# Optimization experiments

Measured on AMD Instinct MI355X. Metric: run time of the kernel, lower is better.

The kernel has to match this reference:

```python
import jax, jax.numpy as jnp
import numpy as np

IDIM = 128   # idim == odim (fc1 input dim must match shift-slice width idim_q)
HDIM = 1024
CDIM = 256
IGNORE_OUT = 10000.0


def setup_inputs() -> dict:
    key = jax.random.key(0)
    ks = jax.random.split(key, 4)
    B, T = 4, 512
    x = jax.random.normal(ks[0], (B, T, IDIM), dtype=jnp.float32)
    y = jax.random.normal(ks[1], (B, T, IDIM), dtype=jnp.float32)
    # xavier-ish init for the two linears (bias zeroed, as in initialize())
    w1 = jax.random.normal(ks[2], (HDIM, IDIM), dtype=jnp.float32) / np.sqrt(IDIM).astype(np.float32)
    b1 = jnp.zeros((HDIM,), jnp.float32)
    w2 = jax.random.normal(ks[3], (IDIM, HDIM), dtype=jnp.float32) / np.sqrt(HDIM).astype(np.float32)
    b2 = jnpts = jnp.zeros((IDIM,), jnp.float32)
    return {"x": x, "y": y, "w1": w1, "b1": b1, "w2": w2, "b2": b2}


def _shift_stack(key_seq, idim):
    """Vectorized _pad_for_shift: (B,T,idim) -> (B,T,2*idim-1,idim) shifted slices."""
    pad = idim - 1
    kp = jnp.pad(key_seq, ((0, 0), (0, 0), (pad, pad)))  # (B,T,3*idim-2)
    idx = jnp.arange(2 * idim - 1)[:, None] + jnp.arange(idim)[None, :]  # (S, idim)
    return kp[..., idx]  # (B,T,S,idim)


def _forward(x, y, w1, b1, w2, b2):
    idim = IDIM
    n_iter = HDIM // CDIM
    seq_mask = (y == IGNORE_OUT)                      # (B,T,odim)
    denom = jnp.sum(~seq_mask).astype(x.dtype)
    y_res, x_res = y, x
    losses = []
    for i in range(n_iter):
        # --- argaug (scale=False): sliding cosine cross-correlation + argmax ---
        kpt = _shift_stack(x_res, idim)               # (B,T,S,idim), S=2*idim-1
        num = jnp.einsum('btd,btsd->bts', y_res, kpt)
        den = jnp.linalg.norm(y_res, axis=-1)[..., None] * jnp.linalg.norm(kpt, axis=-1)
        sim = jnp.where(den == 0, 0.0, num / jnp.where(den == 0, 1.0, den))  # NaN(0/0) -> 0
        idx = jnp.argmax(sim, axis=-1)                # (B,T), first max like torch.max
        x_aug = jnp.take_along_axis(kpt, idx[..., None, None], axis=2)[..., 0, :]  # (B,T,idim)
        # --- attention (detached) ---
        attn = jax.lax.stop_gradient(jax.nn.softmax(x_aug * y_res, axis=-1))
        x_attn = x_aug * attn
        # --- _reverse_pad_for_shift: un-shift x_attn by 2*idim-2 - idx ---
        pad = idim - 1
        xap = jnp.pad(x_attn, ((0, 0), (0, 0), (pad, pad)))
        ridx = (2 * idim - 2 - idx)[..., None] + jnp.arange(idim)  # (B,T,idim)
        x_ele = jnp.take_along_axis(xap, ridx, axis=-1)
        # --- channel-masked two-layer MLP ---
        h = x_attn @ w1.T + b1                        # (B,T,hdim)
        m = jnp.zeros((HDIM,), x.dtype).at[i * CDIM:(i + 1) * CDIM].set(1.0)
        y_ele = (h * m) @ w2.T + b2                   # (B,T,odim)
        # --- masked MSE (sum of masked squared errors / #unmasked) ---
        sq = jnp.where(seq_mask, 0.0, (y_ele - y_res) ** 2)
        losses.append(jnp.sum(sq) / denom)
        y_res = y_res - y_ele
        x_res = x_res - x_ele
    return jnp.mean(jnp.stack(losses))


def reference(x, y, w1, b1, w2, b2):
    return _forward(x, y, w1, b1, w2, b2)
```

## Files before the change

kernel.cpp:

```cpp
#include <hip/hip_runtime.h>
#include <math.h>

#define NBLK  2048
#define NITER 4
#define IGNORE_OUT 10000.0f
#define LOG2E 1.44269504088896340736f

__device__ __forceinline__ float readlanef(float v, int lane){
  return __int_as_float(__builtin_amdgcn_readlane(__float_as_int(v), lane));
}

__device__ __forceinline__ float waveScanInc(float v){
  v += __int_as_float(__builtin_amdgcn_update_dpp(0, __float_as_int(v), 0x111, 0xF, 0xF, true));
  v += __int_as_float(__builtin_amdgcn_update_dpp(0, __float_as_int(v), 0x112, 0xF, 0xF, true));
  v += __int_as_float(__builtin_amdgcn_update_dpp(0, __float_as_int(v), 0x114, 0xF, 0xF, true));
  v += __int_as_float(__builtin_amdgcn_update_dpp(0, __float_as_int(v), 0x118, 0xF, 0xF, true));
  v += __int_as_float(__builtin_amdgcn_update_dpp(0, __float_as_int(v), 0x142, 0xA, 0xF, true));
  v += __int_as_float(__builtin_amdgcn_update_dpp(0, __float_as_int(v), 0x143, 0xC, 0xF, true));
  return v;
}
__device__ __forceinline__ float waveSum(float v){
  return readlanef(waveScanInc(v), 63);
}
__device__ __forceinline__ void waveArgmax(float &v, int &i){
#define AMSTEP(ctrl, rm) { \
    float ov = __int_as_float(__builtin_amdgcn_update_dpp(__float_as_int(v), __float_as_int(v), ctrl, rm, 0xF, false)); \
    int   oi = __builtin_amdgcn_update_dpp(i, i, ctrl, rm, 0xF, false); \
    bool take = (ov > v) || (ov == v && oi < i); \
    v = take ? ov : v; i = take ? oi : i; }
  AMSTEP(0x111, 0xF) AMSTEP(0x112, 0xF) AMSTEP(0x114, 0xF)
  AMSTEP(0x118, 0xF) AMSTEP(0x142, 0xA) AMSTEP(0x143, 0xC)
#undef AMSTEP
  v = readlanef(v, 63);
  i = __builtin_amdgcn_readlane(i, 63);
}
__device__ __forceinline__ void gatherPair(float v0, float v1, int idx, float &a, float &b){
  int c = idx & 63;
  float g0 = __shfl(v0, c, 64);
  float g1 = __shfl(v1, c, 64);
  a = ((unsigned)idx < 128u) ? ((idx & 64) ? g1 : g0) : 0.f;
  int idx2 = idx + 64;
  b = ((unsigned)idx2 < 128u) ? ((idx2 & 64) ? g1 : g0) : 0.f;
}

__global__ __launch_bounds__(256)
void prepK(const float* __restrict__ w1, const float* __restrict__ b1,
           const float* __restrict__ w2, const float* __restrict__ b2,
           float* __restrict__ M4, float* __restrict__ biasT, int* __restrict__ ticket){
  const int blk = blockIdx.x;
  const int tid = threadIdx.x;
  const int u = tid & 127, h = tid >> 7;
  __shared__ float part[256];
  if (blk < 512){
    int i = blk >> 7, o = blk & 127;
    const float* w1p = w1 + (i * 256 + h * 128) * 128 + u;
    const float* w2p = w2 + o * 1024 + i * 256 + h * 128;
    float a0 = 0.f, a1 = 0.f, a2 = 0.f, a3 = 0.f;
    #pragma unroll 8
    for (int c = 0; c < 128; c += 4){
      a0 = fmaf(w1p[(c + 0) * 128], w2p[c + 0], a0);
      a1 = fmaf(w1p[(c + 1) * 128], w2p[c + 1], a1);
      a2 = fmaf(w1p[(c + 2) * 128], w2p[c + 2], a2);
      a3 = fmaf(w1p[(c + 3) * 128], w2p[c + 3], a3);
    }
    part[tid] = (a0 + a1) + (a2 + a3);
    __syncthreads();
    if (h == 0) M4[i * 16384 + (u >> 2) * 512 + o * 4 + (u & 3)] = part[u] + part[128 + u];
  } else if (blk < 516){
    int i = blk - 512;
    const float* w2p = w2 + u * 1024 + i * 256 + h * 128;
    const float* b1p = b1 + i * 256 + h * 128;
    float a0 = h ? 0.f : b2[u], a1 = 0.f, a2 = 0.f, a3 = 0.f;
    #pragma unroll 8
    for (int c = 0; c < 128; c += 4){
      a0 = fmaf(b1p[c + 0], w2p[c + 0], a0);
      a1 = fmaf(b1p[c + 1], w2p[c + 1], a1);
      a2 = fmaf(b1p[c + 2], w2p[c + 2], a2);
      a3 = fmaf(b1p[c + 3], w2p[c + 3], a3);
    }
    part[tid] = (a0 + a1) + (a2 + a3);
    __syncthreads();
    if (h == 0) biasT[i * 128 + u] = part[u] + part[128 + u];
  } else {
    if (tid == 0) *ticket = 0;
  }
}

#define MLD(d0, d1, d2, d3, gg) \
  d0 = Mp[((gg) * 4 + 0) * 128 + u]; d1 = Mp[((gg) * 4 + 1) * 128 + u]; \
  d2 = Mp[((gg) * 4 + 2) * 128 + u]; d3 = Mp[((gg) * 4 + 3) * 128 + u];
#define MFM(m0, m1, m2, m3, src, kb) \
  a0 = fmaf((m0).x, readlanef(src, (kb) + 0), a0);  a0 = fmaf((m0).y, readlanef(src, (kb) + 1), a0); \
  a0 = fmaf((m0).z, readlanef(src, (kb) + 2), a0);  a0 = fmaf((m0).w, readlanef(src, (kb) + 3), a0); \
  a1 = fmaf((m1).x, readlanef(src, (kb) + 4), a1);  a1 = fmaf((m1).y, readlanef(src, (kb) + 5), a1); \
  a1 = fmaf((m1).z, readlanef(src, (kb) + 6), a1);  a1 = fmaf((m1).w, readlanef(src, (kb) + 7), a1); \
  a2 = fmaf((m2).x, readlanef(src, (kb) + 8), a2);  a2 = fmaf((m2).y, readlanef(src, (kb) + 9), a2); \
  a2 = fmaf((m2).z, readlanef(src, (kb) +10), a2);  a2 = fmaf((m2).w, readlanef(src, (kb) +11), a2); \
  a3 = fmaf((m3).x, readlanef(src, (kb) +12), a3);  a3 = fmaf((m3).y, readlanef(src, (kb) +13), a3); \
  a3 = fmaf((m3).z, readlanef(src, (kb) +14), a3);  a3 = fmaf((m3).w, readlanef(src, (kb) +15), a3);

__global__ __launch_bounds__(128, 4)
void mainK(const float* __restrict__ x, const float* __restrict__ y,
           const float* __restrict__ M4, const float* __restrict__ biasT,
           unsigned long long* __restrict__ partials, int* __restrict__ ticket,
           float* __restrict__ out){
  __shared__ float yd[384];
  __shared__ float sVal[2];
  __shared__ int   sIdx[2];
  __shared__ float sL[2], sC[2];
  __shared__ int   sOld;

  const int u = threadIdx.x;
  const int l = u & 63;
  const int w = u >> 6;
  const long base = (long)blockIdx.x * 128;

  float xlo = x[base + l], xhi = x[base + 64 + l];
  float ylo = y[base + l], yhi = y[base + 64 + l];
  const float yOwn0 = w ? yhi : ylo;
  const bool mOwn = (yOwn0 == IGNORE_OUT);
  float cnt = mOwn ? 0.f : 1.f;
  float lossAcc = 0.f;

  yd[128 + u] = yOwn0; yd[256 + u] = yOwn0;
  __syncthreads();

  for (int i = 0; i < NITER; ++i){
    const float4* Mp = (const float4*)(M4 + (size_t)i * 16384);

    float own2 = w ? xhi * xhi : xlo * xlo;
    float oth2 = w ? xlo * xlo : xhi * xhi;
    float v = waveScanInc(own2);
    float osum  = waveSum(oth2);
    float total = readlanef(v, 63) + osum;
    float pref_t = w ? (v + osum) : v;
    float ny2 = waveSum(ylo * ylo + yhi * yhi);

    const float* wp = yd + (255 - u);
    float s0=0.f,s1=0.f,s2=0.f,s3=0.f;
    float t0=0.f,t1=0.f,t2=0.f,t3=0.f;
    float p0=0.f,p1=0.f,p2=0.f,p3=0.f;
    if (w == 0){
      #pragma unroll
      for (int j = 0; j < 64; j += 4){
        float wv0 = wp[j], wv1 = wp[j+1], wv2 = wp[j+2], wv3 = wp[j+3];
        float x0 = readlanef(xlo, j),   x1 = readlanef(xlo, j+1);
        float x2 = readlanef(xlo, j+2), x3 = readlanef(xlo, j+3);
        s0 = fmaf(wv0, x0, s0); s1 = fmaf(wv1, x1, s1);
        s2 = fmaf(wv2, x2, s2); s3 = fmaf(wv3, x3, s3);
        p0 = fmaf((l >= j    ) ? wv0 : 0.f, x0, p0);
        p1 = fmaf((l >= j + 1) ? wv1 : 0.f, x1, p1);
        p2 = fmaf((l >= j + 2) ? wv2 : 0.f, x2, p2);
        p3 = fmaf((l >= j + 3) ? wv3 : 0.f, x3, p3);
      }
      #pragma unroll
      for (int j = 0; j < 64; j += 4){
        float wv0 = wp[64+j], wv1 = wp[64+j+1], wv2 = wp[64+j+2], wv3 = wp[64+j+3];
        t0 = fmaf(wv0, readlanef(xhi, j),   t0);
        t1 = fmaf(wv1, readlanef(xhi, j+1), t1);
        t2 = fmaf(wv2, readlanef(xhi, j+2), t2);
        t3 = fmaf(wv3, readlanef(xhi, j+3), t3);
      }
    } else {
      #pragma unroll
      for (int j = 0; j < 64; j += 4){
        float wv0 = wp[j], wv1 = wp[j+1], wv2 = wp[j+2], wv3 = wp[j+3];
        s0 = fmaf(wv0, readlanef(xlo, j),   s0);
        s1 = fmaf(wv1, readlanef(xlo, j+1), s1);
        s2 = fmaf(wv2, readlanef(xlo, j+2), s2);
        s3 = fmaf(wv3, readlanef(xlo, j+3), s3);
      }
      #pragma unroll
      for (int j = 0; j < 64; j += 4){
        float wv0 = wp[64+j], wv1 = wp[64+j+1], wv2 = wp[64+j+2], wv3 = wp[64+j+3];
        float x0 = readlanef(xhi, j),   x1 = readlanef(xhi, j+1);
        float x2 = readlanef(xhi, j+2), x3 = readlanef(xhi, j+3);
        t0 = fmaf(wv0, x0, t0); t1 = fmaf(wv1, x1, t1);
        t2 = fmaf(wv2, x2, t2); t3 = fmaf(wv3, x3, t3);
        p0 = fmaf((l >= j    ) ? wv0 : 0.f, x0, p0);
        p1 = fmaf((l >= j + 1) ? wv1 : 0.f, x1, p1);
        p2 = fmaf((l >= j + 2) ? wv2 : 0.f, x2, p2);
        p3 = fmaf((l >= j + 3) ? wv3 : 0.f, x3, p3);
      }
    }
    float Sh0 = (s0 + s1) + (s2 + s3);
    float Sh1 = (t0 + t1) + (t2 + t3);
    float P   = (p0 + p1) + (p2 + p3);
    float nt = Sh0 + Sh1;
    float n1 = w ? (Sh0 + P) : P;

    {
      bool yz = (ny2 == 0.f);
      float rNY = __builtin_amdgcn_rsqf(ny2);
      float nx2b = fmaxf(total - pref_t, 0.f);
      float s1v = (yz || pref_t == 0.f) ? 0.f : n1 * __builtin_amdgcn_rsqf(pref_t) * rNY;
      float s2v = (yz || nx2b  == 0.f) ? 0.f : (nt - n1) * __builtin_amdgcn_rsqf(nx2b) * rNY;
      if (u == 127) s2v = -INFINITY;
      float bv = s1v; int bi = u;
      if (s2v > bv){ bv = s2v; bi = u + 128; }
      waveArgmax(bv, bi);
      if (l == 0){ sVal[w] = bv; sIdx[w] = bi; }
    }
    __syncthreads();

    float4 A0, A1, A2, A3, B0, B1, B2, B3;
    MLD(A0, A1, A2, A3, 0)
    MLD(B0, B1, B2, B3, 1)
    float bias_i = biasT[i * 128 + u];

    int sstar;
    {
      float v0 = sVal[0], v1 = sVal[1];
      int   i0 = sIdx[0], i1 = sIdx[1];
      sstar = (v1 > v0 || (v1 == v0 && i1 < i0)) ? i1 : i0;
    }

    float xa, xb;
    gatherPair(xlo, xhi, sstar + l - 127, xa, xb);
    float ea = __builtin_amdgcn_exp2f(xa * ylo * LOG2E);
    float eb = __builtin_amdgcn_exp2f(xb * yhi * LOG2E);
    float rse = __builtin_amdgcn_rcpf(waveSum(ea + eb));
    float wlo = xa * (ea * rse), whi = xb * (eb * rse);

    {
      float ga, gb;
      gatherPair(wlo, whi, l + 127 - sstar, ga, gb);
      xlo -= ga; xhi -= gb;
    }

    float ye;
    {
      float a0 = 0.f, a1 = 0.f, a2 = 0.f, a3 = 0.f;
      MFM(A0, A1, A2, A3, wlo, 0)   MLD(A0, A1, A2, A3, 2)
      MFM(B0, B1, B2, B3, wlo, 16)  MLD(B0, B1, B2, B3, 3)
      MFM(A0, A1, A2, A3, wlo, 32)  MLD(A0, A1, A2, A3, 4)
      MFM(B0, B1, B2, B3, wlo, 48)  MLD(B0, B1, B2, B3, 5)
      MFM(A0, A1, A2, A3, whi, 0)   MLD(A0, A1, A2, A3, 6)
      MFM(B0, B1, B2, B3, whi, 16)  MLD(B0, B1, B2, B3, 7)
      MFM(A0, A1, A2, A3, whi, 32)
      MFM(B0, B1, B2, B3, whi, 48)
      ye = ((a0 + a1) + (a2 + a3)) + bias_i;
    }

    {
      float yOwn = w ? yhi : ylo;
      float df = ye - yOwn;
      if (!mOwn) lossAcc = fmaf(df, df, lossAcc);
      float yNew = yOwn - ye;
      yd[128 + u] = yNew; yd[256 + u] = yNew;
    }
    __syncthreads();
    ylo = yd[128 + l];
    yhi = yd[192 + l];
  }

  lossAcc = waveSum(lossAcc);
  cnt     = waveSum(cnt);
  if (l == 0){ sL[w] = lossAcc; sC[w] = cnt; }
  __syncthreads();
  if (u == 0){
    union { float2 f; unsigned long long v; } pk;
    pk.f.x = sL[0] + sL[1];
    pk.f.y = sC[0] + sC[1];
    __hip_atomic_store(&partials[blockIdx.x], pk.v, __ATOMIC_RELEASE, __HIP_MEMORY_SCOPE_AGENT);
    sOld = __hip_atomic_fetch_add(ticket, 1, __ATOMIC_ACQ_REL, __HIP_MEMORY_SCOPE_AGENT);
  }
  __syncthreads();
  if (sOld == NBLK - 1){
    float ls = 0.f, cs = 0.f;
    for (int g = u; g < NBLK; g += 128){
      union { float2 f; unsigned long long v; } pk;
      pk.v = __hip_atomic_load(&partials[g], __ATOMIC_ACQUIRE, __HIP_MEMORY_SCOPE_AGENT);
      ls += pk.f.x; cs += pk.f.y;
    }
    ls = waveSum(ls); cs = waveSum(cs);
    if (l == 0){ sL[w] = ls; sC[w] = cs; }
    __syncthreads();
    if (u == 0) out[0] = (sL[0] + sL[1]) / ((float)NITER * (sC[0] + sC[1]));
  }
}

extern "C" void kernel_launch(void* const* d_in, const int* in_sizes, int n_in,
                              void* d_out, int out_size, void* d_ws, size_t ws_size,
                              hipStream_t stream){
  const float* x  = (const float*)d_in[0];
  const float* y  = (const float*)d_in[1];
  const float* w1 = (const float*)d_in[2];
  const float* b1 = (const float*)d_in[3];
  const float* w2 = (const float*)d_in[4];
  const float* b2 = (const float*)d_in[5];
  float* out = (float*)d_out;

  int*   ticket = (int*)d_ws;
  float* M4     = (float*)((char*)d_ws + 256);
  float* biasT  = (float*)((char*)d_ws + 256 + 4 * 128 * 128 * sizeof(float));
  unsigned long long* partials =
      (unsigned long long*)((char*)d_ws + 256 + 4 * 128 * 128 * sizeof(float) + 4 * 128 * sizeof(float));

  prepK<<<517, 256, 0, stream>>>(w1, b1, w2, b2, M4, biasT, ticket);
  mainK<<<NBLK, 128, 0, stream>>>(x, y, M4, biasT, partials, ticket, out);
}
```

Baseline: 155.7 us.

## Split each row's correlation and MLP across four waves instead of two

Each block now has 256 threads (four waves) per row instead of 128. The cross-correlation work is split into four 64-lane quarter-sums that are combined through shared memory, and every wave then runs the argmax redundantly, which removes one barrier. The MLP mat-vec is split along the K dimension across wave pairs and reduced through shared memory. This halves the serial work per wave to shorten per-row latency, at the cost of more threads, extra LDS traffic and redundant y/argmax computation in every wave.

```diff
diff --git a/kernel.cpp b/kernel.cpp
--- a/kernel.cpp
+++ b/kernel.cpp
@@ -87,8 +87,8 @@
 }
 
 #define MLD(d0, d1, d2, d3, gg) \
-  d0 = Mp[((gg) * 4 + 0) * 128 + u]; d1 = Mp[((gg) * 4 + 1) * 128 + u]; \
-  d2 = Mp[((gg) * 4 + 2) * 128 + u]; d3 = Mp[((gg) * 4 + 3) * 128 + u];
+  d0 = MpW[((gg) * 4 + 0) * 128]; d1 = MpW[((gg) * 4 + 1) * 128]; \
+  d2 = MpW[((gg) * 4 + 2) * 128]; d3 = MpW[((gg) * 4 + 3) * 128];
 #define MFM(m0, m1, m2, m3, src, kb) \
   a0 = fmaf((m0).x, readlanef(src, (kb) + 0), a0);  a0 = fmaf((m0).y, readlanef(src, (kb) + 1), a0); \
   a0 = fmaf((m0).z, readlanef(src, (kb) + 2), a0);  a0 = fmaf((m0).w, readlanef(src, (kb) + 3), a0); \
@@ -99,53 +99,49 @@
   a3 = fmaf((m3).x, readlanef(src, (kb) +12), a3);  a3 = fmaf((m3).y, readlanef(src, (kb) +13), a3); \
   a3 = fmaf((m3).z, readlanef(src, (kb) +14), a3);  a3 = fmaf((m3).w, readlanef(src, (kb) +15), a3);
 
-__global__ __launch_bounds__(128, 4)
+__global__ __launch_bounds__(256, 8)
 void mainK(const float* __restrict__ x, const float* __restrict__ y,
            const float* __restrict__ M4, const float* __restrict__ biasT,
            unsigned long long* __restrict__ partials, int* __restrict__ ticket,
            float* __restrict__ out){
-  __shared__ float yd[384];
-  __shared__ float sVal[2];
-  __shared__ int   sIdx[2];
-  __shared__ float sL[2], sC[2];
+  __shared__ float ydW[4][384];
+  __shared__ float Ab[64], Bb[64], Cb[64], Db[64], Pb[64], Qb[64];
+  __shared__ float mlpB[256];
+  __shared__ float sL[4], sC[4];
   __shared__ int   sOld;
 
-  const int u = threadIdx.x;
-  const int l = u & 63;
-  const int w = u >> 6;
+  const int u  = threadIdx.x;
+  const int l  = u & 63;
+  const int w  = u >> 6;
+  const int th = w & 1;
+  const int jh = w >> 1;
+  const int o  = u & 127;
   const long base = (long)blockIdx.x * 128;
 
   float xlo = x[base + l], xhi = x[base + 64 + l];
   float ylo = y[base + l], yhi = y[base + 64 + l];
-  const float yOwn0 = w ? yhi : ylo;
-  const bool mOwn = (yOwn0 == IGNORE_OUT);
-  float cnt = mOwn ? 0.f : 1.f;
+  const bool mask_l = (ylo == IGNORE_OUT);
+  const bool mask_h = (yhi == IGNORE_OUT);
+  float cnt = (w == 0) ? (mask_l ? 0.f : 1.f) : ((w == 1) ? (mask_h ? 0.f : 1.f) : 0.f);
   float lossAcc = 0.f;
 
-  yd[128 + u] = yOwn0; yd[256 + u] = yOwn0;
-  __syncthreads();
+  float* ydw = ydW[w];
+  ydw[128 + l] = ylo; ydw[192 + l] = yhi; ydw[256 + l] = ylo; ydw[320 + l] = yhi;
+  const float* wp = ydw + (255 - 64 * th + 64 * jh) - l;
 
   for (int i = 0; i < NITER; ++i){
-    const float4* Mp = (const float4*)(M4 + (size_t)i * 16384);
-
-    float own2 = w ? xhi * xhi : xlo * xlo;
-    float oth2 = w ? xlo * xlo : xhi * xhi;
-    float v = waveScanInc(own2);
-    float osum  = waveSum(oth2);
-    float total = readlanef(v, 63) + osum;
-    float pref_t = w ? (v + osum) : v;
-    float ny2 = waveSum(ylo * ylo + yhi * yhi);
-
-    const float* wp = yd + (255 - u);
-    float s0=0.f,s1=0.f,s2=0.f,s3=0.f;
-    float t0=0.f,t1=0.f,t2=0.f,t3=0.f;
-    float p0=0.f,p1=0.f,p2=0.f,p3=0.f;
-    if (w == 0){
+    const float4* MpW = (const float4*)(M4 + (size_t)i * 16384) + jh * 2048 + o;
+    float bias_l = biasT[i * 128 + l];
+    float bias_h = biasT[i * 128 + 64 + l];
+
+    const float xsrc = jh ? xhi : xlo;
+    float s0=0.f,s1=0.f,s2=0.f,s3=0.f, p0=0.f,p1=0.f,p2=0.f,p3=0.f;
+    if (w == 0 || w == 3){
       #pragma unroll
       for (int j = 0; j < 64; j += 4){
         float wv0 = wp[j], wv1 = wp[j+1], wv2 = wp[j+2], wv3 = wp[j+3];
-        float x0 = readlanef(xlo, j),   x1 = readlanef(xlo, j+1);
-        float x2 = readlanef(xlo, j+2), x3 = readlanef(xlo, j+3);
+        float x0 = readlanef(xsrc, j),   x1 = readlanef(xsrc, j+1);
+        float x2 = readlanef(xsrc, j+2), x3 = readlanef(xsrc, j+3);
         s0 = fmaf(wv0, x0, s0); s1 = fmaf(wv1, x1, s1);
         s2 = fmaf(wv2, x2, s2); s3 = fmaf(wv3, x3, s3);
         p0 = fmaf((l >= j    ) ? wv0 : 0.f, x0, p0);
@@ -153,67 +149,59 @@
         p2 = fmaf((l >= j + 2) ? wv2 : 0.f, x2, p2);
         p3 = fmaf((l >= j + 3) ? wv3 : 0.f, x3, p3);
       }
-      #pragma unroll
-      for (int j = 0; j < 64; j += 4){
-        float wv0 = wp[64+j], wv1 = wp[64+j+1], wv2 = wp[64+j+2], wv3 = wp[64+j+3];
-        t0 = fmaf(wv0, readlanef(xhi, j),   t0);
-        t1 = fmaf(wv1, readlanef(xhi, j+1), t1);
-        t2 = fmaf(wv2, readlanef(xhi, j+2), t2);
-        t3 = fmaf(wv3, readlanef(xhi, j+3), t3);
-      }
     } else {
       #pragma unroll
       for (int j = 0; j < 64; j += 4){
         float wv0 = wp[j], wv1 = wp[j+1], wv2 = wp[j+2], wv3 = wp[j+3];
-        s0 = fmaf(wv0, readlanef(xlo, j),   s0);
-        s1 = fmaf(wv1, readlanef(xlo, j+1), s1);
-        s2 = fmaf(wv2, readlanef(xlo, j+2), s2);
-        s3 = fmaf(wv3, readlanef(xlo, j+3), s3);
+        s0 = fmaf(wv0, readlanef(xsrc, j),   s0);
+        s1 = fmaf(wv1, readlanef(xsrc, j+1), s1);
+        s2 = fmaf(wv2, readlanef(xsrc, j+2), s2);
+        s3 = fmaf(wv3, readlanef(xsrc, j+3), s3);
       }
-      #pragma unroll
-      for (int j = 0; j < 64; j += 4){
-        float wv0 = wp[64+j], wv1 = wp[64+j+1], wv2 = wp[64+j+2], wv3 = wp[64+j+3];
-        float x0 = readlanef(xhi, j),   x1 = readlanef(xhi, j+1);
-        float x2 = readlanef(xhi, j+2), x3 = readlanef(xhi, j+3);
-        t0 = fmaf(wv0, x0, t0); t1 = fmaf(wv1, x1, t1);
-        t2 = fmaf(wv2, x2, t2); t3 = fmaf(wv3, x3, t3);
-        p0 = fmaf((l >= j    ) ? wv0 : 0.f, x0, p0);
-        p1 = fmaf((l >= j + 1) ? wv1 : 0.f, x1, p1);
-        p2 = fmaf((l >= j + 2) ? wv2 : 0.f, x2, p2);
-        p3 = fmaf((l >= j + 3) ? wv3 : 0.f, x3, p3);
-      }
-    }
-    float Sh0 = (s0 + s1) + (s2 + s3);
-    float Sh1 = (t0 + t1) + (t2 + t3);
-    float P   = (p0 + p1) + (p2 + p3);
-    float nt = Sh0 + Sh1;
-    float n1 = w ? (Sh0 + P) : P;
-
+    }
+    float S = (s0 + s1) + (s2 + s3);
+    float P = (p0 + p1) + (p2 + p3);
+    if      (w == 0){ Ab[l] = S; Pb[l] = P; }
+    else if (w == 1){ Bb[l] = S; }
+    else if (w == 2){ Cb[l] = S; }
+    else            { Db[l] = S; Qb[l] = P; }
+
+    float v_lo = waveScanInc(xlo * xlo);
+    float slo  = readlanef(v_lo, 63);
+    float v_hi = waveScanInc(xhi * xhi);
+    float shi  = readlanef(v_hi, 63);
+    float total = slo + shi;
+    float ny2 = waveSum(ylo * ylo + yhi * yhi);
+
+    __syncthreads();
+
+    float SA = Ab[l], SB = Bb[l], SC = Cb[l], SD = Db[l], PP = Pb[l], QQ = Qb[l];
+    float nt_l = SA + SC, n1_l = PP;
+    float nt_h = SB + SD, n1_h = SB + QQ;
+    float pref_l = v_lo;
+    float pref_h = v_hi + slo;
+    int sstar;
     {
       bool yz = (ny2 == 0.f);
       float rNY = __builtin_amdgcn_rsqf(ny2);
-      float nx2b = fmaxf(total - pref_t, 0.f);
-      float s1v = (yz || pref_t == 0.f) ? 0.f : n1 * __builtin_amdgcn_rsqf(pref_t) * rNY;
-      float s2v = (yz || nx2b  == 0.f) ? 0.f : (nt - n1) * __builtin_amdgcn_rsqf(nx2b) * rNY;
-      if (u == 127) s2v = -INFINITY;
-      float bv = s1v; int bi = u;
-      if (s2v > bv){ bv = s2v; bi = u + 128; }
+      float nx_l = fmaxf(total - pref_l, 0.f);
+      float nx_h = fmaxf(total - pref_h, 0.f);
+      float s1l = (yz || pref_l == 0.f) ? 0.f : n1_l * __builtin_amdgcn_rsqf(pref_l) * rNY;
+      float s2l = (yz || nx_l   == 0.f) ? 0.f : (nt_l - n1_l) * __builtin_amdgcn_rsqf(nx_l) * rNY;
+      float s1h = (yz || pref_h == 0.f) ? 0.f : n1_h * __builtin_amdgcn_rsqf(pref_h) * rNY;
+      float s2h = (yz || nx_h   == 0.f) ? 0.f : (nt_h - n1_h) * __builtin_amdgcn_rsqf(nx_h) * rNY;
+      if (l == 63) s2h = -INFINITY;
+      float bv = s1l; int bi = l;
+      if (s1h > bv){ bv = s1h; bi = 64 + l; }
+      if (s2l > bv){ bv = s2l; bi = 128 + l; }
+      if (s2h > bv){ bv = s2h; bi = 192 + l; }
       waveArgmax(bv, bi);
-      if (l == 0){ sVal[w] = bv; sIdx[w] = bi; }
-    }
-    __syncthreads();
+      sstar = bi;
+    }
 
     float4 A0, A1, A2, A3, B0, B1, B2, B3;
     MLD(A0, A1, A2, A3, 0)
     MLD(B0, B1, B2, B3, 1)
-    float bias_i = biasT[i * 128 + u];
-
-    int sstar;
-    {
-      float v0 = sVal[0], v1 = sVal[1];
-      int   i0 = sIdx[0], i1 = sIdx[1];
-      sstar = (v1 > v0 || (v1 == v0 && i1 < i0)) ? i1 : i0;
-    }
 
     float xa, xb;
     gatherPair(xlo, xhi, sstar + l - 127, xa, xb);
@@ -221,37 +209,32 @@
     float eb = __builtin_amdgcn_exp2f(xb * yhi * LOG2E);
     float rse = __builtin_amdgcn_rcpf(waveSum(ea + eb));
     float wlo = xa * (ea * rse), whi = xb * (eb * rse);
-
     {
       float ga, gb;
       gatherPair(wlo, whi, l + 127 - sstar, ga, gb);
       xlo -= ga; xhi -= gb;
     }
 
-    float ye;
-    {
+    {
+      const float wsrc = jh ? whi : wlo;
       float a0 = 0.f, a1 = 0.f, a2 = 0.f, a3 = 0.f;
-      MFM(A0, A1, A2, A3, wlo, 0)   MLD(A0, A1, A2, A3, 2)
-      MFM(B0, B1, B2, B3, wlo, 16)  MLD(B0, B1, B2, B3, 3)
-      MFM(A0, A1, A2, A3, wlo, 32)  MLD(A0, A1, A2, A3, 4)
-      MFM(B0, B1, B2, B3, wlo, 48)  MLD(B0, B1, B2, B3, 5)
-      MFM(A0, A1, A2, A3, whi, 0)   MLD(A0, A1, A2, A3, 6)
-      MFM(B0, B1, B2, B3, whi, 16)  MLD(B0, B1, B2, B3, 7)
-      MFM(A0, A1, A2, A3, whi, 32)
-      MFM(B0, B1, B2, B3, whi, 48)
-      ye = ((a0 + a1) + (a2 + a3)) + bias_i;
-    }
-
-    {
-      float yOwn = w ? yhi : ylo;
-      float df = ye - yOwn;
-      if (!mOwn) lossAcc = fmaf(df, df, lossAcc);
-      float yNew = yOwn - ye;
-      yd[128 + u] = yNew; yd[256 + u] = yNew;
-    }
-    __syncthreads();
-    ylo = yd[128 + l];
-    yhi = yd[192 + l];
+      MFM(A0, A1, A2, A3, wsrc, 0)   MLD(A0, A1, A2, A3, 2)
+      MFM(B0, B1, B2, B3, wsrc, 16)  MLD(B0, B1, B2, B3, 3)
+      MFM(A0, A1, A2, A3, wsrc, 32)
+      MFM(B0, B1, B2, B3, wsrc, 48)
+      mlpB[u] = (a0 + a1) + (a2 + a3);
+    }
+    __syncthreads();
+
+    {
+      float ye_l = (mlpB[l]      + mlpB[128 + l]) + bias_l;
+      float ye_h = (mlpB[64 + l] + mlpB[192 + l]) + bias_h;
+      float df_l = ye_l - ylo, df_h = ye_h - yhi;
+      if (w == 0 && !mask_l) lossAcc = fmaf(df_l, df_l, lossAcc);
+      if (w == 1 && !mask_h) lossAcc = fmaf(df_h, df_h, lossAcc);
+      ylo -= ye_l; yhi -= ye_h;
+      ydw[128 + l] = ylo; ydw[192 + l] = yhi; ydw[256 + l] = ylo; ydw[320 + l] = yhi;
+    }
   }
 
   lossAcc = waveSum(lossAcc);
@@ -260,15 +243,15 @@
   __syncthreads();
   if (u == 0){
     union { float2 f; unsigned long long v; } pk;
-    pk.f.x = sL[0] + sL[1];
-    pk.f.y = sC[0] + sC[1];
+    pk.f.x = (sL[0] + sL[1]) + (sL[2] + sL[3]);
+    pk.f.y = (sC[0] + sC[1]) + (sC[2] + sC[3]);
     __hip_atomic_store(&partials[blockIdx.x], pk.v, __ATOMIC_RELEASE, __HIP_MEMORY_SCOPE_AGENT);
     sOld = __hip_atomic_fetch_add(ticket, 1, __ATOMIC_ACQ_REL, __HIP_MEMORY_SCOPE_AGENT);
   }
   __syncthreads();
   if (sOld == NBLK - 1){
     float ls = 0.f, cs = 0.f;
-    for (int g = u; g < NBLK; g += 128){
+    for (int g = u; g < NBLK; g += 256){
       union { float2 f; unsigned long long v; } pk;
       pk.v = __hip_atomic_load(&partials[g], __ATOMIC_ACQUIRE, __HIP_MEMORY_SCOPE_AGENT);
       ls += pk.f.x; cs += pk.f.y;
@@ -276,7 +259,8 @@
     ls = waveSum(ls); cs = waveSum(cs);
     if (l == 0){ sL[w] = ls; sC[w] = cs; }
     __syncthreads();
-    if (u == 0) out[0] = (sL[0] + sL[1]) / ((float)NITER * (sC[0] + sC[1]));
+    if (u == 0) out[0] = ((sL[0] + sL[1]) + (sL[2] + sL[3])) /
+                         ((float)NITER * ((sC[0] + sC[1]) + (sC[2] + sC[3])));
   }
 }
 
@@ -298,5 +282,5 @@
       (unsigned long long*)((char*)d_ws + 256 + 4 * 128 * 128 * sizeof(float) + 4 * 128 * sizeof(float));
 
   prepK<<<517, 256, 0, stream>>>(w1, b1, w2, b2, M4, biasT, ticket);
-  mainK<<<NBLK, 128, 0, stream>>>(x, y, M4, biasT, partials, ticket, out);
-}
+  mainK<<<NBLK, 256, 0, stream>>>(x, y, M4, biasT, partials, ticket, out);
+}
```

New measurement: 164.8 us. 5.9% more time.
